# Kernel tuning notes

Hardware: AMD Instinct MI355X
Metric: run time of the kernel (lower is better)

The kernel has to match this reference:

```python
import jax, jax.numpy as jnp
import numpy as np

B, T, F = 32, 2048, 16
C = F + 1      # input channels (time prepended)
H = 64         # output_dims: latent CDE state size
HH = 64        # hidden_dims: vector-field MLP width
DEPTH = 4      # num_hidden_layers -> DEPTH-1 inner linears
INIT = 64      # intial_dims


def _lin(k, fan_in, shape):
    b = 1.0 / np.sqrt(fan_in)
    return jax.random.uniform(k, shape, jnp.float32, -b, b)


def setup_inputs() -> dict:
    key = jax.random.key(0)
    ks = jax.random.split(key, 15)
    return {
        "x": jax.random.normal(ks[0], (B, T, F), jnp.float32),
        # z0 initializer MLP: Linear(C,INIT) -> ReLU -> Linear(INIT,H)
        "wi1": _lin(ks[1], C, (C, INIT)), "bi1": _lin(ks[2], C, (INIT,)),
        "wi2": _lin(ks[3], INIT, (INIT, H)), "bi2": _lin(ks[4], INIT, (H,)),
        # CDEFunc
        "w_in": _lin(ks[5], H, (H, HH)), "b_in": _lin(ks[6], H, (HH,)),
        "w_hid": _lin(ks[7], HH, (DEPTH - 1, HH, HH)), "b_hid": _lin(ks[8], HH, (DEPTH - 1, HH)),
        "w_out": _lin(ks[9], HH, (HH, C * H)), "b_out": _lin(ks[10], HH, (C * H,)),
        # output projection Linear(H, F)
        "w_proj": _lin(ks[11], H, (H, F)), "b_proj": _lin(ks[12], H, (F,)),
    }


def _cde_f(z, w_in, b_in, w_hid, b_hid, w_out, b_out):
    # CDEFunc.forward: MLP -> tanh, reshaped to (b, H, C)
    h = jax.nn.relu(z @ w_in + b_in)
    for i in range(w_hid.shape[0]):
        h = jax.nn.relu(h @ w_hid[i] + b_hid[i])
    return jnp.tanh((h @ w_out + b_out).reshape(z.shape[0], H, C))


def _forward(x, wi1, bi1, wi2, bi2, w_in, b_in, w_hid, b_hid, w_out, b_out, w_proj, b_proj):
    b, t_len, _ = x.shape
    t = jnp.arange(t_len, dtype=x.dtype)
    xa = jnp.concatenate([jnp.broadcast_to(t[None, :, None], (b, t_len, 1)), x], axis=-1)  # (b,T,C)

    # Hermite cubic with backward differences (torchcde): knot derivs are backward
    # diffs with the first repeated; on interval i (h=1):
    #   X'(s) = d_i + 2*c_i*s + 3*e_i*s^2,  c_i = 3*dx - 2*d_i - d_{i+1},  e_i = -2*dx + d_i + d_{i+1}
    diffs = xa[:, 1:] - xa[:, :-1]                      # (b,T-1,C)
    d = jnp.concatenate([diffs[:, :1], diffs], axis=1)  # (b,T,C)
    di, dip1 = d[:, :-1], d[:, 1:]
    cc = 3.0 * diffs - 2.0 * di - dip1
    ee = -2.0 * diffs + di + dip1

    def deriv(s):
        return di + (2.0 * s) * cc + (3.0 * s * s) * ee  # (b,T-1,C)

    # torchdiffeq 'rk4' = 3/8-rule: evals at s = 0, 1/3, 2/3, 1 within each unit interval
    xdots = jnp.stack([deriv(0.0), deriv(1.0 / 3.0), deriv(2.0 / 3.0), deriv(1.0)], axis=0)
    xdots = jnp.moveaxis(xdots, 2, 0)  # (T-1, 4, b, C)

    z0 = jax.nn.relu(xa[:, 0] @ wi1 + bi1) @ wi2 + bi2  # (b,H)

    def g(z, xd):
        f = _cde_f(z, w_in, b_in, w_hid, b_hid, w_out, b_out)  # (b,H,C)
        return jnp.einsum('bhc,bc->bh', f, xd)

    def step(z, xd4):
        k1 = g(z, xd4[0])
        k2 = g(z + k1 / 3.0, xd4[1])
        k3 = g(z + (k2 - k1 / 3.0), xd4[2])
        k4 = g(z + (k1 - k2 + k3), xd4[3])
        zn = z + (k1 + 3.0 * (k2 + k3) + k4) * 0.125
        return zn, zn

    _, zs = jax.lax.scan(step, z0, xdots)                # (T-1,b,H)
    z_T = jnp.moveaxis(jnp.concatenate([z0[None], zs], axis=0), 0, 1)  # (b,T,H)

    # act -> dropout (eval: identity) -> output_layer
    out = jax.nn.gelu(z_T, approximate=False) @ w_proj + b_proj        # (b,T,F)
    return z_T, out


def reference(x, wi1, bi1, wi2, bi2, w_in, b_in, w_hid, b_hid, w_out, b_out, w_proj, b_proj):
    z_T, out = _forward(x, wi1, bi1, wi2, bi2, w_in, b_in, w_hid, b_hid, w_out, b_out, w_proj, b_proj)
    not_mask = jnp.zeros((x.shape[0], x.shape[1]), dtype=bool)  # mask='all_true' (eval mode)
    return z_T, out, not_mask
```

## Files before the change

kernel.cpp:

```cpp
#include <hip/hip_runtime.h>
#include <math.h>

#define BB 32
#define TT 2048
#define FF 16
#define CC 17
#define HH 64

typedef float v2f __attribute__((ext_vector_type(2)));
typedef float v4f __attribute__((ext_vector_type(4)));
typedef _Float16 h2 __attribute__((ext_vector_type(2)));

__device__ __forceinline__ float rl(float v, int lane) {
    return __int_as_float(__builtin_amdgcn_readlane(__float_as_int(v), lane));
}
__device__ __forceinline__ unsigned rlu(unsigned v, int lane) {
    return (unsigned)__builtin_amdgcn_readlane((int)v, lane);
}
__device__ __forceinline__ float uf(float v) {
    return __int_as_float(__builtin_amdgcn_readfirstlane(__float_as_int(v)));
}
__device__ __forceinline__ float ftanh(float x) {
    float e = __builtin_amdgcn_exp2f(x * 2.88539008177792681472f);
    return 1.0f - 2.0f * __builtin_amdgcn_rcpf(e + 1.0f);
}
__device__ __forceinline__ float fdot2u(unsigned a, unsigned b, float c) {
    return __builtin_amdgcn_fdot2(__builtin_bit_cast(h2, a),
                                  __builtin_bit_cast(h2, b), c, false);
}
__device__ __forceinline__ unsigned packw(float a, float b) {
    h2 p; p.x = (_Float16)(a * 256.0f); p.y = (_Float16)(b * 256.0f);
    return __builtin_bit_cast(unsigned, p);
}
__device__ __forceinline__ void bar_lds() {
    asm volatile("s_waitcnt lgkmcnt(0)\n\ts_barrier" ::: "memory");
}
#define PIN(v) asm volatile("" : "+v"(v))

__attribute__((amdgpu_waves_per_eu(2, 2)))
__launch_bounds__(512)
__global__ void ncde_main(const float* __restrict__ x,
                          const float* __restrict__ wi1, const float* __restrict__ bi1,
                          const float* __restrict__ wi2, const float* __restrict__ bi2,
                          const float* __restrict__ w_in, const float* __restrict__ b_in,
                          const float* __restrict__ w_hid, const float* __restrict__ b_hid,
                          const float* __restrict__ w_out, const float* __restrict__ b_out,
                          float* __restrict__ zT)
{
    const int b   = blockIdx.x;
    const int tid = threadIdx.x;
    const int w   = tid >> 6;
    const int l   = tid & 63;

    __shared__ float pht[4][64][12];
    __shared__ float pgqt[64][20];

    const int cs = w ^ ((l >> 3) & 7);

    unsigned whp[4][4];
    #pragma unroll
    for (int kk = 0; kk < 4; ++kk) {
        int k = 8 * w + 2 * kk;
        whp[0][kk] = packw(w_in[k * HH + l],               w_in[(k + 1) * HH + l]);
        whp[1][kk] = packw(w_hid[(0 * HH + k) * HH + l],   w_hid[(0 * HH + k + 1) * HH + l]);
        whp[2][kk] = packw(w_hid[(1 * HH + k) * HH + l],   w_hid[(1 * HH + k + 1) * HH + l]);
        whp[3][kk] = packw(w_hid[(2 * HH + k) * HH + l],   w_hid[(2 * HH + k + 1) * HH + l]);
    }
    float bfold[4];
    bfold[0] = (w == 0) ? b_in[l] : 0.0f;
    bfold[1] = (w == 0) ? b_hid[0 * HH + l] : 0.0f;
    bfold[2] = (w == 0) ? b_hid[1 * HH + l] : 0.0f;
    bfold[3] = (w == 0) ? b_hid[2 * HH + l] : 0.0f;

    const int c0 = 2 * w, c1 = 2 * w + 1;
    unsigned wo0p[32], wo1p[32], w16p[4];
    #pragma unroll
    for (int j = 0; j < 32; ++j) {
        wo0p[j] = packw(w_out[(2 * j) * (CC * HH) + l * CC + c0],
                        w_out[(2 * j + 1) * (CC * HH) + l * CC + c0]);
        wo1p[j] = packw(w_out[(2 * j) * (CC * HH) + l * CC + c1],
                        w_out[(2 * j + 1) * (CC * HH) + l * CC + c1]);
    }
    #pragma unroll
    for (int jj = 0; jj < 4; ++jj)
        w16p[jj] = packw(w_out[(8 * w + 2 * jj) * (CC * HH) + l * CC + 16],
                         w_out[(8 * w + 2 * jj + 1) * (CC * HH) + l * CC + 16]);
    float bo0  = b_out[l * CC + c0];
    float bo1  = b_out[l * CC + c1];
    float bo16 = (w == 0) ? b_out[l * CC + 16] : 0.0f;

    #pragma unroll
    for (int j = 0; j < 32; ++j) { PIN(wo0p[j]); PIN(wo1p[j]); }
    #pragma unroll
    for (int jj = 0; jj < 4; ++jj) PIN(w16p[jj]);
    #pragma unroll
    for (int lay = 0; lay < 4; ++lay) {
        PIN(whp[lay][0]); PIN(whp[lay][1]); PIN(whp[lay][2]); PIN(whp[lay][3]);
    }
    PIN(bo0); PIN(bo1); PIN(bo16);

    float z;
    {
        float h0 = bi1[l];
        #pragma unroll
        for (int c = 1; c < CC; ++c)
            h0 = fmaf(x[(size_t)b * TT * FF + (c - 1)], wi1[c * HH + l], h0);
        h0 = fmaxf(h0, 0.0f);
        z = bi2[l];
        #pragma unroll
        for (int k = 0; k < 64; ++k)
            z = fmaf(rl(h0, k), wi2[k * HH + l], z);
    }
    if (w == 0) zT[(size_t)b * TT * HH + l] = z;

    auto packb = [&](float v) -> unsigned {
        float hs = v * 0.00390625f;
        float pr = __shfl_xor(hs, 1);
        float a  = (l & 1) ? pr : hs;
        float bb = (l & 1) ? hs : pr;
        return __builtin_bit_cast(unsigned, __builtin_amdgcn_cvt_pkrtz(a, bb));
    };

    auto G = [&](float zin, float xd0, float xd1, float xd16) -> float {
        float cur = zin;
        #pragma unroll
        for (int L = 0; L < 4; ++L) {
            unsigned hp = packb(cur);
            float a0 = bfold[L], a1 = 0.0f;
            a0 = fdot2u(rlu(hp, 8 * w + 0), whp[L][0], a0);
            a1 = fdot2u(rlu(hp, 8 * w + 2), whp[L][1], a1);
            a0 = fdot2u(rlu(hp, 8 * w + 4), whp[L][2], a0);
            a1 = fdot2u(rlu(hp, 8 * w + 6), whp[L][3], a1);
            pht[L][l][cs] = a0 + a1;
            bar_lds();
            const float* row = &pht[L][l][0];
            v4f q0 = *reinterpret_cast<const v4f*>(row);
            v4f q1 = *reinterpret_cast<const v4f*>(row + 4);
            float hsum = ((q0.x + q0.y) + (q0.z + q0.w)) + ((q1.x + q1.y) + (q1.z + q1.w));
            cur = fmaxf(hsum, 0.0f);
        }
        unsigned hp = packb(cur);
        float u0a = 0.f, u0b = 0.f, u1a = 0.f, u1b = 0.f;
        #pragma unroll
        for (int j = 0; j < 32; j += 2) {
            unsigned s0 = rlu(hp, 2 * j);
            unsigned s1 = rlu(hp, 2 * j + 2);
            u0a = fdot2u(s0, wo0p[j],     u0a);
            u1a = fdot2u(s0, wo1p[j],     u1a);
            u0b = fdot2u(s1, wo0p[j + 1], u0b);
            u1b = fdot2u(s1, wo1p[j + 1], u1b);
        }
        float a16a = bo16, a16b = 0.f;
        #pragma unroll
        for (int jj = 0; jj < 4; jj += 2) {
            unsigned s0 = rlu(hp, 8 * w + 2 * jj);
            unsigned s1 = rlu(hp, 8 * w + 2 * jj + 2);
            a16a = fdot2u(s0, w16p[jj],     a16a);
            a16b = fdot2u(s1, w16p[jj + 1], a16b);
        }
        float pg = ftanh(u0a + u0b + bo0) * xd0 + ftanh(u1a + u1b + bo1) * xd1;
        *reinterpret_cast<v2f*>(&pgqt[l][2 * cs]) = (v2f){ pg, a16a + a16b };
        bar_lds();
        const float* prow = &pgqt[l][0];
        v4f r0 = *reinterpret_cast<const v4f*>(prow);
        v4f r1 = *reinterpret_cast<const v4f*>(prow + 4);
        v4f r2 = *reinterpret_cast<const v4f*>(prow + 8);
        v4f r3 = *reinterpret_cast<const v4f*>(prow + 12);
        float pgs  = ((r0.x + r0.z) + (r1.x + r1.z)) + ((r2.x + r2.z) + (r3.x + r3.z));
        float a16s = ((r0.y + r0.w) + (r1.y + r1.w)) + ((r2.y + r2.w) + (r3.y + r3.w));
        return fmaf(ftanh(a16s), xd16, pgs);
    };

    const float* xb = x + (size_t)b * TT * FF;
    const bool hasc0 = (w != 0);
    const int  f0 = 2 * w - 1;
    const int  f1 = 2 * w;
    float xp0  = hasc0 ? uf(xb[f0]) : 0.0f;
    float xp1  = uf(xb[f1]);
    float xp16 = uf(xb[15]);
    float xn0  = hasc0 ? uf(xb[FF + f0]) : 0.0f;
    float xn1  = uf(xb[FF + f1]);
    float xn16 = uf(xb[FF + 15]);
    float dc0  = hasc0 ? (xn0 - xp0) : 1.0f;
    float dc1  = xn1 - xp1;
    float dc16 = xn16 - xp16;
    float dp0 = dc0, dp1 = dc1, dp16 = dc16;
    xp0 = xn0; xp1 = xn1; xp16 = xn16;

    #pragma unroll 1
    for (int t = 0; t < TT - 1; ++t) {
        const float f43 = 4.0f / 3.0f;
        float x20  = dp0  + f43 * (dc0  - dp0);
        float x21  = dp1  + f43 * (dc1  - dp1);
        float x216 = dp16 + f43 * (dc16 - dp16);

        int tn = (t + 2 < TT) ? (t + 2) : (TT - 1);
        float yn0  = hasc0 ? uf(xb[tn * FF + f0]) : 0.0f;
        float yn1  = uf(xb[tn * FF + f1]);
        float yn16 = uf(xb[tn * FF + 15]);

        float k1 = G(z, dp0, dp1, dp16);
        float k2 = G(z + k1 * (1.0f / 3.0f), dc0, dc1, dc16);
        float k3 = G(z + (k2 - k1 * (1.0f / 3.0f)), x20, x21, x216);
        float k4 = G(z + (k1 - k2 + k3), dc0, dc1, dc16);
        z = z + 0.125f * (k1 + 3.0f * (k2 + k3) + k4);

        if (w == 0) zT[((size_t)b * TT + t + 1) * HH + l] = z;

        dp0 = dc0; dp1 = dc1; dp16 = dc16;
        dc0 = hasc0 ? (yn0 - xp0) : 1.0f;
        dc1 = yn1 - xp1;
        dc16 = yn16 - xp16;
        xp0 = yn0; xp1 = yn1; xp16 = yn16;
    }
}

__global__ void ncde_proj(const float* __restrict__ zT,
                          const float* __restrict__ w_proj, const float* __restrict__ b_proj,
                          float* __restrict__ out, float* __restrict__ mask)
{
    __shared__ float gz[16][64];
    const int blk = blockIdx.x;
    const int tid = threadIdx.x;
    const int r16 = tid >> 4, f = tid & 15;
    const int row0 = blk * 16;

    #pragma unroll
    for (int i = 0; i < 4; ++i) {
        int idx = tid + i * 256;
        int r = idx >> 6, k = idx & 63;
        float zv = zT[(size_t)(row0 + r) * HH + k];
        gz[r][k] = 0.5f * zv * (1.0f + erff(zv * 0.70710678118654752f));
    }
    __syncthreads();

    float acc = b_proj[f];
    #pragma unroll
    for (int k = 0; k < 64; ++k)
        acc = fmaf(gz[r16][k], w_proj[k * FF + f], acc);
    out[(size_t)(row0 + r16) * FF + f] = acc;
    if (f == 0) mask[row0 + r16] = 0.0f;
}

extern "C" void kernel_launch(void* const* d_in, const int* in_sizes, int n_in,
                              void* d_out, int out_size, void* d_ws, size_t ws_size,
                              hipStream_t stream)
{
    (void)in_sizes; (void)n_in; (void)d_ws; (void)ws_size; (void)out_size;
    const float* x      = (const float*)d_in[0];
    const float* wi1    = (const float*)d_in[1];
    const float* bi1    = (const float*)d_in[2];
    const float* wi2    = (const float*)d_in[3];
    const float* bi2    = (const float*)d_in[4];
    const float* w_in   = (const float*)d_in[5];
    const float* b_in   = (const float*)d_in[6];
    const float* w_hid  = (const float*)d_in[7];
    const float* b_hid  = (const float*)d_in[8];
    const float* w_out  = (const float*)d_in[9];
    const float* b_out  = (const float*)d_in[10];
    const float* w_proj = (const float*)d_in[11];
    const float* b_proj = (const float*)d_in[12];

    float* zT   = (float*)d_out;
    float* outp = zT + (size_t)BB * TT * HH;
    float* mask = outp + (size_t)BB * TT * FF;

    ncde_main<<<dim3(BB), dim3(512), 0, stream>>>(
        x, wi1, bi1, wi2, bi2, w_in, b_in, w_hid, b_hid, w_out, b_out, zT);
    ncde_proj<<<dim3((BB * TT) / 16), dim3(256), 0, stream>>>(
        zT, w_proj, b_proj, outp, mask);
}
```

Baseline: 12.86 ms.

## Compute hidden MLP layers in a single wave to cut per-layer barriers

Moves the four hidden-layer matvecs from an 8-wave split with LDS reductions and a barrier per layer to a single wave that reads fp16-packed weights from LDS. The resulting hidden vector is broadcast via LDS, leaving two barriers per vector-field evaluation instead of five. The output layer now reads the packed activations from LDS with vector loads instead of readlanes. In exchange, the serial work on wave 0 grows substantially while the other waves wait.

```diff
diff --git a/kernel.cpp b/kernel.cpp
--- a/kernel.cpp
+++ b/kernel.cpp
@@ -9,6 +9,8 @@
 
 typedef float v2f __attribute__((ext_vector_type(2)));
 typedef float v4f __attribute__((ext_vector_type(4)));
+typedef unsigned v2u __attribute__((ext_vector_type(2)));
+typedef unsigned v4u __attribute__((ext_vector_type(4)));
 typedef _Float16 h2 __attribute__((ext_vector_type(2)));
 
 __device__ __forceinline__ float rl(float v, int lane) {
@@ -52,25 +54,22 @@
     const int w   = tid >> 6;
     const int l   = tid & 63;
 
-    __shared__ float pht[4][64][12];
+    __shared__ unsigned WLds[4 * 64 * 34];
+    __shared__ __align__(16) unsigned hb16[32];
     __shared__ float pgqt[64][20];
 
     const int cs = w ^ ((l >> 3) & 7);
 
-    unsigned whp[4][4];
-    #pragma unroll
-    for (int kk = 0; kk < 4; ++kk) {
-        int k = 8 * w + 2 * kk;
-        whp[0][kk] = packw(w_in[k * HH + l],               w_in[(k + 1) * HH + l]);
-        whp[1][kk] = packw(w_hid[(0 * HH + k) * HH + l],   w_hid[(0 * HH + k + 1) * HH + l]);
-        whp[2][kk] = packw(w_hid[(1 * HH + k) * HH + l],   w_hid[(1 * HH + k + 1) * HH + l]);
-        whp[3][kk] = packw(w_hid[(2 * HH + k) * HH + l],   w_hid[(2 * HH + k + 1) * HH + l]);
-    }
-    float bfold[4];
-    bfold[0] = (w == 0) ? b_in[l] : 0.0f;
-    bfold[1] = (w == 0) ? b_hid[0 * HH + l] : 0.0f;
-    bfold[2] = (w == 0) ? b_hid[1 * HH + l] : 0.0f;
-    bfold[3] = (w == 0) ? b_hid[2 * HH + l] : 0.0f;
+    for (int i = tid; i < 4 * 64 * 32; i += 512) {
+        int L = i >> 11, r = i & 2047, col = r >> 5, j = r & 31;
+        float wa, wb;
+        if (L == 0) { wa = w_in[(2 * j) * HH + col];     wb = w_in[(2 * j + 1) * HH + col]; }
+        else { wa = w_hid[((L - 1) * HH + 2 * j) * HH + col];
+               wb = w_hid[((L - 1) * HH + 2 * j + 1) * HH + col]; }
+        WLds[L * (64 * 34) + col * 34 + j] = packw(wa, wb);
+    }
+
+    float bh[4] = { b_in[l], b_hid[l], b_hid[HH + l], b_hid[2 * HH + l] };
 
     const int c0 = 2 * w, c1 = 2 * w + 1;
     unsigned wo0p[32], wo1p[32], w16p[4];
@@ -93,10 +92,6 @@
     for (int j = 0; j < 32; ++j) { PIN(wo0p[j]); PIN(wo1p[j]); }
     #pragma unroll
     for (int jj = 0; jj < 4; ++jj) PIN(w16p[jj]);
-    #pragma unroll
-    for (int lay = 0; lay < 4; ++lay) {
-        PIN(whp[lay][0]); PIN(whp[lay][1]); PIN(whp[lay][2]); PIN(whp[lay][3]);
-    }
     PIN(bo0); PIN(bo1); PIN(bo16);
 
     float z;
@@ -111,7 +106,8 @@
         for (int k = 0; k < 64; ++k)
             z = fmaf(rl(h0, k), wi2[k * HH + l], z);
     }
-    if (w == 0) zT[(size_t)b * TT * HH + l] = z;
+    if (w == 7) zT[(size_t)b * TT * HH + l] = z;
+    __syncthreads();
 
     auto packb = [&](float v) -> unsigned {
         float hs = v * 0.00390625f;
@@ -122,43 +118,54 @@
     };
 
     auto G = [&](float zin, float xd0, float xd1, float xd16) -> float {
-        float cur = zin;
+        if (w == 0) {
+            float cur = zin;
+            #pragma unroll
+            for (int L = 0; L < 4; ++L) {
+                const unsigned* WL = &WLds[L * (64 * 34) + l * 34];
+                unsigned hp = packb(cur);
+                v2u wr[16];
+                #pragma unroll
+                for (int r = 0; r < 4; ++r)
+                    wr[r] = *reinterpret_cast<const v2u*>(&WL[2 * r]);
+                float a0 = bh[L], a1 = 0.f, a2 = 0.f, a3 = 0.f;
+                #pragma unroll
+                for (int r = 0; r < 16; ++r) {
+                    if (r + 4 < 16)
+                        wr[r + 4] = *reinterpret_cast<const v2u*>(&WL[2 * (r + 4)]);
+                    unsigned sx = rlu(hp, 4 * r);
+                    unsigned sy = rlu(hp, 4 * r + 2);
+                    if (r & 1) { a2 = fdot2u(sx, wr[r].x, a2); a3 = fdot2u(sy, wr[r].y, a3); }
+                    else       { a0 = fdot2u(sx, wr[r].x, a0); a1 = fdot2u(sy, wr[r].y, a1); }
+                }
+                cur = fmaxf((a0 + a1) + (a2 + a3), 0.0f);
+            }
+            unsigned hp = packb(cur);
+            if ((l & 1) == 0) hb16[l >> 1] = hp;
+        }
+        bar_lds();
+
+        float u0a = 0.f, u0b = 0.f, u0c = 0.f, u0d = 0.f;
+        float u1a = 0.f, u1b = 0.f, u1c = 0.f, u1d = 0.f;
         #pragma unroll
-        for (int L = 0; L < 4; ++L) {
-            unsigned hp = packb(cur);
-            float a0 = bfold[L], a1 = 0.0f;
-            a0 = fdot2u(rlu(hp, 8 * w + 0), whp[L][0], a0);
-            a1 = fdot2u(rlu(hp, 8 * w + 2), whp[L][1], a1);
-            a0 = fdot2u(rlu(hp, 8 * w + 4), whp[L][2], a0);
-            a1 = fdot2u(rlu(hp, 8 * w + 6), whp[L][3], a1);
-            pht[L][l][cs] = a0 + a1;
-            bar_lds();
-            const float* row = &pht[L][l][0];
-            v4f q0 = *reinterpret_cast<const v4f*>(row);
-            v4f q1 = *reinterpret_cast<const v4f*>(row + 4);
-            float hsum = ((q0.x + q0.y) + (q0.z + q0.w)) + ((q1.x + q1.y) + (q1.z + q1.w));
-            cur = fmaxf(hsum, 0.0f);
+        for (int j = 0; j < 8; ++j) {
+            v4u q = *reinterpret_cast<const v4u*>(&hb16[4 * j]);
+            u0a = fdot2u(q.x, wo0p[4 * j + 0], u0a);
+            u0b = fdot2u(q.y, wo0p[4 * j + 1], u0b);
+            u0c = fdot2u(q.z, wo0p[4 * j + 2], u0c);
+            u0d = fdot2u(q.w, wo0p[4 * j + 3], u0d);
+            u1a = fdot2u(q.x, wo1p[4 * j + 0], u1a);
+            u1b = fdot2u(q.y, wo1p[4 * j + 1], u1b);
+            u1c = fdot2u(q.z, wo1p[4 * j + 2], u1c);
+            u1d = fdot2u(q.w, wo1p[4 * j + 3], u1d);
         }
-        unsigned hp = packb(cur);
-        float u0a = 0.f, u0b = 0.f, u1a = 0.f, u1b = 0.f;
-        #pragma unroll
-        for (int j = 0; j < 32; j += 2) {
-            unsigned s0 = rlu(hp, 2 * j);
-            unsigned s1 = rlu(hp, 2 * j + 2);
-            u0a = fdot2u(s0, wo0p[j],     u0a);
-            u1a = fdot2u(s0, wo1p[j],     u1a);
-            u0b = fdot2u(s1, wo0p[j + 1], u0b);
-            u1b = fdot2u(s1, wo1p[j + 1], u1b);
-        }
-        float a16a = bo16, a16b = 0.f;
-        #pragma unroll
-        for (int jj = 0; jj < 4; jj += 2) {
-            unsigned s0 = rlu(hp, 8 * w + 2 * jj);
-            unsigned s1 = rlu(hp, 8 * w + 2 * jj + 2);
-            a16a = fdot2u(s0, w16p[jj],     a16a);
-            a16b = fdot2u(s1, w16p[jj + 1], a16b);
-        }
-        float pg = ftanh(u0a + u0b + bo0) * xd0 + ftanh(u1a + u1b + bo1) * xd1;
+        v4u qc = *reinterpret_cast<const v4u*>(&hb16[4 * w]);
+        float a16a = fdot2u(qc.x, w16p[0], fdot2u(qc.z, w16p[2], bo16));
+        float a16b = fdot2u(qc.y, w16p[1], fdot2u(qc.w, w16p[3], 0.0f));
+
+        float u0 = ((u0a + u0b) + (u0c + u0d)) + bo0;
+        float u1 = ((u1a + u1b) + (u1c + u1d)) + bo1;
+        float pg = ftanh(u0) * xd0 + ftanh(u1) * xd1;
         *reinterpret_cast<v2f*>(&pgqt[l][2 * cs]) = (v2f){ pg, a16a + a16b };
         bar_lds();
         const float* prow = &pgqt[l][0];
@@ -205,7 +212,7 @@
         float k4 = G(z + (k1 - k2 + k3), dc0, dc1, dc16);
         z = z + 0.125f * (k1 + 3.0f * (k2 + k3) + k4);
 
-        if (w == 0) zT[((size_t)b * TT + t + 1) * HH + l] = z;
+        if (w == 7) zT[((size_t)b * TT + t + 1) * HH + l] = z;
 
         dp0 = dc0; dp1 = dc1; dp16 = dc16;
         dc0 = hasc0 ? (yn0 - xp0) : 1.0f;
```

After: 13.29 ms. 1.03x slower.
